# Kernel tuning notes

Measured on AMD Instinct MI355X. Metric: run time of the kernel, lower is better.

Reference implementation:

```python
import jax, jax.numpy as jnp
import numpy as np

EMBED_DIM = 512
NUM_HEADS = 8
HEAD_DIM = EMBED_DIM // NUM_HEADS
B, N, M = 4, 4096, 4096


def setup_inputs() -> dict:
    key = jax.random.key(0)
    ks = jax.random.split(key, 16)
    s = 0.02
    inp = {
        "query": jax.random.normal(ks[0], (B, N, EMBED_DIM), jnp.float32),
        "key": jax.random.normal(ks[1], (B, M, EMBED_DIM), jnp.float32),
        "value": jax.random.normal(ks[2], (B, M, EMBED_DIM), jnp.float32),
        # Linear weights stored as (in, out) so y = x @ W + b (== torch x @ W.T + b)
        "Wq": jax.random.normal(ks[3], (EMBED_DIM, EMBED_DIM), jnp.float32) * s,
        "bq": jnp.zeros((EMBED_DIM,), jnp.float32),
        "Wk": jax.random.normal(ks[4], (EMBED_DIM, EMBED_DIM), jnp.float32) * s,
        "bk": jnp.zeros((EMBED_DIM,), jnp.float32),
        "Wv": jax.random.normal(ks[5], (EMBED_DIM, EMBED_DIM), jnp.float32) * s,
        "bv": jnp.zeros((EMBED_DIM,), jnp.float32),
        # rank expansion MLP acts per-head on head_dim
        "W1": jax.random.normal(ks[6], (HEAD_DIM, HEAD_DIM * 2), jnp.float32) * s,
        "b1": jnp.zeros((HEAD_DIM * 2,), jnp.float32),
        "W2": jax.random.normal(ks[7], (HEAD_DIM * 2, HEAD_DIM), jnp.float32) * s,
        "b2": jnp.zeros((HEAD_DIM,), jnp.float32),
        "Wo": jax.random.normal(ks[8], (EMBED_DIM, EMBED_DIM), jnp.float32) * s,
        "bo": jnp.zeros((EMBED_DIM,), jnp.float32),
    }
    return inp


def reference(query, key, value, Wq, bq, Wk, bk, Wv, bv, W1, b1, W2, b2, Wo, bo):
    b, n, _ = query.shape
    m = key.shape[1]
    H, D = NUM_HEADS, HEAD_DIM
    # ELU+1 feature maps on projected q, k
    q = jax.nn.elu(query @ Wq + bq) + 1.0           # [B,N,E]
    k = jax.nn.elu(key @ Wk + bk) + 1.0             # [B,M,E]
    v = value @ Wv + bv                              # [B,M,E]
    q = q.reshape(b, n, H, D)
    k = k.reshape(b, m, H, D)
    v = v.reshape(b, m, H, D)
    # rank expansion MLP on keys (per head_dim), exact GELU as nn.GELU default
    k_aug = jax.nn.gelu(k @ W1 + b1, approximate=False) @ W2 + b2
    k_aug = jax.nn.elu(k_aug) + 1.0                  # [B,M,H,D]
    # inputs already fp32 (torch .float() casts are identity here)
    k_scaled = k_aug / m                             # normalize over context len
    kv_context = jnp.einsum('bmhd,bmhe->bhde', k_scaled, v)   # [B,H,D,D]
    out = jnp.einsum('bnhd,bhde->bnhe', q, kv_context)        # [B,N,H,D]
    k_sum = k_scaled.sum(axis=1)                      # [B,H,D]
    denom = jnp.einsum('bnhd,bhd->bnh', q, k_sum)     # [B,N,H]
    out = out / jnp.clip(denom, 1e-6, None)[..., None]
    out = jnp.clip(jnp.nan_to_num(out, nan=0.0, posinf=65000.0, neginf=-65000.0),
                   -65000.0, 65000.0)
    out = out.reshape(b, n, H * D)
    return out @ Wo + bo
```

## Files before the change

kernel.cpp:

```cpp
#include <hip/hip_runtime.h>
#include <cmath>

#define DEV __device__ __forceinline__

typedef __bf16 bf16x8 __attribute__((ext_vector_type(8)));
typedef float f32x4 __attribute__((ext_vector_type(4)));
typedef unsigned int u32;
typedef unsigned short u16;

DEV u16 f2bf(float f) {
  union { float f; u32 u; } v;
  v.f = f;
  u32 u = v.u;
  u += 0x7fffu + ((u >> 16) & 1u);
  return (u16)(u >> 16);
}

DEV void async16(const void* g, void* l) {
  __builtin_amdgcn_global_load_lds((const __attribute__((address_space(1))) u32*)g,
                                   (__attribute__((address_space(3))) u32*)l, 16, 0, 0);
}

enum { ACT_ID = 0, ACT_ELU1 = 1, ACT_GELU = 2, ACT_ELU1S = 3 };
enum { OM_ROW = 0, OM_VT = 1 };

DEV float apply_act(int ACT, float v, float scale) {
  if (ACT == ACT_ELU1)  return (v > 0.f) ? (v + 1.f) : __expf(v);
  if (ACT == ACT_GELU)  return 0.5f * v * (1.f + erff(v * 0.7071067811865475f));
  if (ACT == ACT_ELU1S) return ((v > 0.f) ? (v + 1.f) : __expf(v)) * scale;
  return v;
}

template <int BM, int BN, int K, int WR, int WC, int ACT, int OBF16, int OMODE, int AFP32>
__global__ __launch_bounds__(256)
void gemm_bf16(const void* __restrict__ Av, const u16* __restrict__ Bt,
               const float* __restrict__ bias, void* __restrict__ Yv,
               int NC, float scale)
{
  constexpr int BI = BN / 64;
  constexpr int SBASE = BM * 32 + BN * 32;
  constexpr int SBSZ = (OMODE == OM_VT && 4 * 64 * 72 > SBASE) ? 4 * 64 * 72 : SBASE;
  __shared__ __align__(16) u16 SB[SBSZ];
  u16* AsU = SB;
  u16* Bs = SB + BM * 32;
  static_assert(WR * WC == 4, "4 waves");

  const int tid = threadIdx.x;
  const int wv = tid >> 6, lane = tid & 63;
  const int wr = wv / WC, wc = wv % WC;
  const int lrow = lane & 15, lq = lane >> 4;
  const int c0 = blockIdx.x * BN;
  const long r0 = (long)blockIdx.y * BM;
  const float* Af = (const float*)Av;
  const u16* Ah = (const u16*)Av;

  f32x4 acc[4][4] = {};

  for (int kt = 0; kt < K; kt += 32) {
    if (AFP32) {
      const int row = tid >> 2, kq = tid & 3;
#pragma unroll
      for (int it = 0; it < BM / 64; ++it) {
        const int r = it * 64 + row;
        const float* g = Af + (r0 + r) * K + kt + kq * 8;
        float4 lo = *(const float4*)g;
        float4 hi = *(const float4*)(g + 4);
        union { ushort4 h[2]; uint4 q; } pk;
        pk.h[0].x = f2bf(lo.x); pk.h[0].y = f2bf(lo.y);
        pk.h[0].z = f2bf(lo.z); pk.h[0].w = f2bf(lo.w);
        pk.h[1].x = f2bf(hi.x); pk.h[1].y = f2bf(hi.y);
        pk.h[1].z = f2bf(hi.z); pk.h[1].w = f2bf(hi.w);
        *(uint4*)&AsU[r * 32 + kq * 8] = pk.q;
      }
    } else {
#pragma unroll
      for (int i = 0; i < BM / 64; ++i) {
        const int s = (wv * (BM / 64) + i) * 64 + lane;
        async16(Ah + (r0 + (s >> 2)) * (long)K + kt + (s & 3) * 8,
                &AsU[(wv * (BM / 64) + i) * 512]);
      }
    }
#pragma unroll
    for (int i = 0; i < BI; ++i) {
      const int s = (wv * BI + i) * 64 + lane;
      async16(Bt + ((long)c0 + (s >> 2)) * K + kt + (s & 3) * 8,
              &Bs[(wv * BI + i) * 512]);
    }
    __syncthreads();
    bf16x8 af[4], bfr[4];
#pragma unroll
    for (int i = 0; i < 4; ++i)
      af[i] = *(const bf16x8*)&AsU[(wr * 64 + i * 16 + lrow) * 32 + lq * 8];
#pragma unroll
    for (int j = 0; j < 4; ++j)
      bfr[j] = *(const bf16x8*)&Bs[(wc * 64 + j * 16 + lrow) * 32 + lq * 8];
#pragma unroll
    for (int i = 0; i < 4; ++i)
#pragma unroll
      for (int j = 0; j < 4; ++j)
        acc[i][j] = __builtin_amdgcn_mfma_f32_16x16x32_bf16(af[i], bfr[j], acc[i][j], 0, 0, 0);
    __syncthreads();
  }

  float* Yf = (float*)Yv;
  u16* Yh = (u16*)Yv;

  if (OMODE == OM_ROW) {
#pragma unroll
    for (int i = 0; i < 4; ++i) {
#pragma unroll
      for (int j = 0; j < 4; ++j) {
        const int col = c0 + wc * 64 + j * 16 + lrow;
        const float bv = bias[col];
#pragma unroll
        for (int p = 0; p < 4; ++p) {
          const float o = apply_act(ACT, acc[i][j][p] + bv, scale);
          const long row = r0 + wr * 64 + i * 16 + lq * 4 + p;
          const long yi = row * NC + col;
          if (OBF16) Yh[yi] = f2bf(o);
          else       Yf[yi] = o;
        }
      }
    }
  } else {
    u16* LTv = SB + wv * 4608;
#pragma unroll
    for (int i = 0; i < 4; ++i) {
#pragma unroll
      for (int j = 0; j < 4; ++j) {
        const int col = c0 + wc * 64 + j * 16 + lrow;
        const float bv = bias[col];
        ushort4 w;
        w.x = f2bf(apply_act(ACT, acc[i][j][0] + bv, scale));
        w.y = f2bf(apply_act(ACT, acc[i][j][1] + bv, scale));
        w.z = f2bf(apply_act(ACT, acc[i][j][2] + bv, scale));
        w.w = f2bf(apply_act(ACT, acc[i][j][3] + bv, scale));
        const int e_l = j * 16 + lrow;
        const int m_l = i * 16 + lq * 4;
        *(ushort4*)&LTv[e_l * 72 + m_l] = w;
      }
    }
    const int b = (int)(r0 >> 12);
    const int h = (c0 + wc * 64) >> 6;
    const int mg0 = (int)(r0 & 4095) + wr * 64;
#pragma unroll
    for (int ps = 0; ps < 8; ++ps) {
      const int e = ps * 8 + (lane >> 3);
      const int mq = (lane & 7) * 8;
      uint4 v = *(const uint4*)&LTv[e * 72 + mq];
      *(uint4*)(Yh + (((long)b * 8 + h) * 64 + e) * 4096 + mg0 + mq) = v;
    }
  }
}

struct TArgs {
  const float* src[6];
  u16* dst[6];
  int K[6];
  int N[6];
};
__global__ __launch_bounds__(256)
void transpose_w(TArgs a)
{
  const int m = blockIdx.z;
  const int K = a.K[m], N = a.N[m];
  const int kt = blockIdx.y * 64, nt = blockIdx.x * 64;
  if (kt >= K || nt >= N) return;
  const float* src = a.src[m];
  u16* dst = a.dst[m];
  __shared__ u16 t[64][72];
  const int tx = threadIdx.x & 15, ty = threadIdx.x >> 4;
#pragma unroll
  for (int rr = 0; rr < 64; rr += 16) {
    const int k = kt + ty + rr;
    float4 v = *(const float4*)(src + (long)k * N + nt + tx * 4);
    t[tx * 4 + 0][ty + rr] = f2bf(v.x);
    t[tx * 4 + 1][ty + rr] = f2bf(v.y);
    t[tx * 4 + 2][ty + rr] = f2bf(v.z);
    t[tx * 4 + 3][ty + rr] = f2bf(v.w);
  }
  __syncthreads();
#pragma unroll
  for (int it = 0; it < 2; ++it) {
    const int s = threadIdx.x + it * 256;
    const int r = s >> 3, c = (s & 7) * 8;
    ushort4 u0 = *(ushort4*)&t[r][c];
    ushort4 u1 = *(ushort4*)&t[r][c + 4];
    *(ushort4*)(dst + (long)(nt + r) * K + kt + c) = u0;
    *(ushort4*)(dst + (long)(nt + r) * K + kt + c + 4) = u1;
  }
}

__global__ __launch_bounds__(256)
void mlp_fused(const u16* __restrict__ kact, const u16* __restrict__ W1T,
               const u16* __restrict__ W2T, const float* __restrict__ b1,
               const float* __restrict__ b2, u16* __restrict__ kaT, float invM)
{
  __shared__ __align__(16) u16 SB[27136];
  u16* As  = SB;
  u16* W1p = SB + 9216;
  u16* W2p = SB + 18432;
  u16* hid = SB;
  u16* LT2 = SB;

  const int tid = threadIdx.x, wv = tid >> 6, lane = tid & 63;
  const int lrow = lane & 15, lq = lane >> 4;
  const int bh = blockIdx.y, b = bh >> 3, h = bh & 7;
  const int m0 = blockIdx.x * 128;
  const long kbase = ((long)b * 4096 + m0) * 512 + h * 64;

#pragma unroll
  for (int i = 0; i < 4; ++i) {
    const int c = i * 256 + tid;
    const int row = c >> 3, p = c & 7;
    uint4 v = *(const uint4*)(kact + kbase + (long)row * 512 + p * 8);
    *(uint4*)&As[row * 72 + p * 8] = v;
  }
#pragma unroll
  for (int i = 0; i < 4; ++i) {
    const int c = i * 256 + tid;
    const int row = c >> 3, p = c & 7;
    uint4 v = *(const uint4*)(W1T + c * 8);
    *(uint4*)&W1p[row * 72 + p * 8] = v;
  }
#pragma unroll
  for (int i = 0; i < 4; ++i) {
    const int c = i * 256 + tid;
    const int row = c >> 4, p = c & 15;
    uint4 v = *(const uint4*)(W2T + c * 8);
    *(uint4*)&W2p[row * 136 + p * 8] = v;
  }
  __syncthreads();

  const int c0 = (wv >> 1) * 64, mh0 = (wv & 1) * 64;
  f32x4 acc1[4][4] = {};
#pragma unroll
  for (int kt = 0; kt < 2; ++kt) {
    bf16x8 wa[4], kb[4];
#pragma unroll
    for (int i = 0; i < 4; ++i)
      wa[i] = *(const bf16x8*)&W1p[(c0 + i * 16 + lrow) * 72 + kt * 32 + lq * 8];
#pragma unroll
    for (int j = 0; j < 4; ++j)
      kb[j] = *(const bf16x8*)&As[(mh0 + j * 16 + lrow) * 72 + kt * 32 + lq * 8];
#pragma unroll
    for (int i = 0; i < 4; ++i)
#pragma unroll
      for (int j = 0; j < 4; ++j)
        acc1[i][j] = __builtin_amdgcn_mfma_f32_16x16x32_bf16(wa[i], kb[j], acc1[i][j], 0, 0, 0);
  }
  __syncthreads();

#pragma unroll
  for (int i = 0; i < 4; ++i) {
    const int cc = c0 + i * 16 + lq * 4;
    float4 bv = *(const float4*)(b1 + cc);
#pragma unroll
    for (int j = 0; j < 4; ++j) {
      const int m = mh0 + j * 16 + lrow;
      float x0 = acc1[i][j][0] + bv.x, x1 = acc1[i][j][1] + bv.y;
      float x2 = acc1[i][j][2] + bv.z, x3 = acc1[i][j][3] + bv.w;
      ushort4 w;
      w.x = f2bf(0.5f * x0 * (1.f + erff(x0 * 0.7071067811865475f)));
      w.y = f2bf(0.5f * x1 * (1.f + erff(x1 * 0.7071067811865475f)));
      w.z = f2bf(0.5f * x2 * (1.f + erff(x2 * 0.7071067811865475f)));
      w.w = f2bf(0.5f * x3 * (1.f + erff(x3 * 0.7071067811865475f)));
      *(ushort4*)&hid[m * 136 + cc] = w;
    }
  }
  __syncthreads();

  const int d0 = (wv >> 1) * 32, mh2 = (wv & 1) * 64;
  f32x4 acc2[4][2] = {};
#pragma unroll
  for (int kt = 0; kt < 4; ++kt) {
    bf16x8 wa[2], hb[4];
#pragma unroll
    for (int i = 0; i < 2; ++i)
      wa[i] = *(const bf16x8*)&W2p[(d0 + i * 16 + lrow) * 136 + kt * 32 + lq * 8];
#pragma unroll
    for (int j = 0; j < 4; ++j)
      hb[j] = *(const bf16x8*)&hid[(mh2 + j * 16 + lrow) * 136 + kt * 32 + lq * 8];
#pragma unroll
    for (int j = 0; j < 4; ++j)
#pragma unroll
      for (int i = 0; i < 2; ++i)
        acc2[j][i] = __builtin_amdgcn_mfma_f32_16x16x32_bf16(hb[j], wa[i], acc2[j][i], 0, 0, 0);
  }
  __syncthreads();

#pragma unroll
  for (int i = 0; i < 2; ++i) {
    const int d = d0 + i * 16 + lrow;
    const float bd = b2[d];
#pragma unroll
    for (int j = 0; j < 4; ++j) {
      const int ml = mh2 + j * 16 + lq * 4;
      ushort4 w;
#pragma unroll
      for (int p = 0; p < 4; ++p) {
        float v = acc2[j][i][p] + bd;
        v = ((v > 0.f) ? (v + 1.f) : __expf(v)) * invM;
        ((u16*)&w)[p] = f2bf(v);
      }
      *(ushort4*)&LT2[d * 136 + ml] = w;
    }
  }
  __syncthreads();
#pragma unroll
  for (int it = 0; it < 4; ++it) {
    const int c = it * 256 + tid;
    const int d = c >> 4, mq = (c & 15) * 8;
    uint4 v = *(const uint4*)&LT2[d * 136 + mq];
    *(uint4*)(kaT + ((long)bh * 64 + d) * 4096 + m0 + mq) = v;
  }
}

__global__ __launch_bounds__(256)
void kv_gemm(const u16* __restrict__ kaT, const u16* __restrict__ vT,
             float* __restrict__ kvp, float* __restrict__ ksp)
{
  const int sp = blockIdx.x;
  const int bh = blockIdx.y;
  __shared__ u16 SB[16384];
  u16* As = SB;
  u16* Bs = SB + 8192;
  const int tid = threadIdx.x, wv = tid >> 6, lane = tid & 63;
  const int lrow = lane & 15, lq = lane >> 4;
  f32x4 acc[4][4] = {};
  f32x4 accs[4] = {};
  bf16x8 ones;
#pragma unroll
  for (int z = 0; z < 8; ++z) ones[z] = (__bf16)1.0f;
  const long base = (long)bh * 64 * 4096;

  for (int ph = 0; ph < 2; ++ph) {
    const int m0 = sp * 256 + ph * 128;
#pragma unroll
    for (int i = 0; i < 4; ++i) {
      const int s = (wv * 4 + i) * 64 + lane;
      const int chunk = s >> 8, row = (s >> 2) & 63, part = s & 3;
      const long g = base + (long)row * 4096 + m0 + chunk * 32 + part * 8;
      async16(kaT + g, &As[(wv * 4 + i) * 512]);
      async16(vT + g, &Bs[(wv * 4 + i) * 512]);
    }
    __syncthreads();
    bf16x8 af[4], bfr[4];
#pragma unroll
    for (int i = 0; i < 4; ++i)
      af[i] = *(const bf16x8*)&As[wv * 2048 + (i * 16 + lrow) * 32 + lq * 8];
#pragma unroll
    for (int j = 0; j < 4; ++j)
      bfr[j] = *(const bf16x8*)&Bs[wv * 2048 + (j * 16 + lrow) * 32 + lq * 8];
#pragma unroll
    for (int i = 0; i < 4; ++i) {
#pragma unroll
      for (int j = 0; j < 4; ++j)
        acc[i][j] = __builtin_amdgcn_mfma_f32_16x16x32_bf16(af[i], bfr[j], acc[i][j], 0, 0, 0);
      accs[i] = __builtin_amdgcn_mfma_f32_16x16x32_bf16(af[i], ones, accs[i], 0, 0, 0);
    }
    __syncthreads();
  }

  float* red = (float*)SB;
  float* ksr = red + 64 * 68;
  for (int w = 0; w < 4; ++w) {
    __syncthreads();
    if (wv == w) {
#pragma unroll
      for (int i = 0; i < 4; ++i) {
#pragma unroll
        for (int j = 0; j < 4; ++j) {
          const int e = j * 16 + lrow, dd = i * 16 + lq * 4;
          float* p = &red[e * 68 + dd];
          if (w == 0) { p[0] = acc[i][j][0]; p[1] = acc[i][j][1]; p[2] = acc[i][j][2]; p[3] = acc[i][j][3]; }
          else        { p[0] += acc[i][j][0]; p[1] += acc[i][j][1]; p[2] += acc[i][j][2]; p[3] += acc[i][j][3]; }
        }
        if (lrow == 0) {
          const int dd = i * 16 + lq * 4;
#pragma unroll
          for (int p2 = 0; p2 < 4; ++p2) {
            if (w == 0) ksr[dd + p2] = accs[i][p2];
            else        ksr[dd + p2] += accs[i][p2];
          }
        }
      }
    }
  }
  __syncthreads();
  float* kvo = kvp + ((long)sp * 32 + bh) * 4096;
  for (int s = tid; s < 4096; s += 256) kvo[s] = red[(s >> 6) * 68 + (s & 63)];
  if (tid < 64) ksp[(sp * 32 + bh) * 64 + tid] = ksr[tid];
}

__global__ __launch_bounds__(256)
void kv_reduce(const float* __restrict__ kvp, const float* __restrict__ ksp,
               u16* __restrict__ kvT, u16* __restrict__ ksumT)
{
  const int bh = blockIdx.x;
  const int t = threadIdx.x;
  for (int s = t; s < 4096; s += 256) {
    float v = 0.f;
#pragma unroll
    for (int sp = 0; sp < 16; ++sp) v += kvp[((long)sp * 32 + bh) * 4096 + s];
    kvT[(long)bh * 4096 + s] = f2bf(v);
  }
  if (t < 64) {
    float v = 0.f;
#pragma unroll
    for (int sp = 0; sp < 16; ++sp) v += ksp[(sp * 32 + bh) * 64 + t];
    ksumT[bh * 64 + t] = f2bf(v);
  }
}

__global__ __launch_bounds__(256)
void attn_mfma(const u16* __restrict__ q, const u16* __restrict__ kvT,
               const u16* __restrict__ ksumT, u16* __restrict__ attn)
{
  __shared__ u16 SB[17408];
  const int tid = threadIdx.x, wv = tid >> 6, lane = tid & 63;
  const int lrow = lane & 15, lq = lane >> 4;
  const int n0 = blockIdx.x * 256;
  const int bh = blockIdx.y, b = bh >> 3, h = bh & 7;
  u16* As = SB;

#pragma unroll
  for (int half = 0; half < 2; ++half)
#pragma unroll
    for (int i = 0; i < 4; ++i) {
      const int s = (wv * 4 + i) * 64 + lane;
      async16(q + ((long)(b * 4096 + n0 + (s >> 2))) * 512 + h * 64 + half * 32 + (s & 3) * 8,
              &As[half * 8192 + (wv * 4 + i) * 512]);
    }
  bf16x8 bfr[2][4], ks[2];
#pragma unroll
  for (int half = 0; half < 2; ++half) {
#pragma unroll
    for (int j = 0; j < 4; ++j)
      bfr[half][j] = *(const bf16x8*)(kvT + ((long)bh * 64 + j * 16 + lrow) * 64 + half * 32 + lq * 8);
    ks[half] = *(const bf16x8*)(ksumT + bh * 64 + half * 32 + lq * 8);
  }
  __syncthreads();

  f32x4 acc[4][4] = {};
  f32x4 accd[4] = {};
#pragma unroll
  for (int half = 0; half < 2; ++half) {
    bf16x8 af[4];
#pragma unroll
    for (int i = 0; i < 4; ++i)
      af[i] = *(const bf16x8*)&As[half * 8192 + (wv * 64 + i * 16 + lrow) * 32 + lq * 8];
#pragma unroll
    for (int i = 0; i < 4; ++i) {
#pragma unroll
      for (int j = 0; j < 4; ++j)
        acc[i][j] = __builtin_amdgcn_mfma_f32_16x16x32_bf16(af[i], bfr[half][j], acc[i][j], 0, 0, 0);
      accd[i] = __builtin_amdgcn_mfma_f32_16x16x32_bf16(af[i], ks[half], accd[i], 0, 0, 0);
    }
  }
  __syncthreads();

  u16* LT = SB;
#pragma unroll
  for (int i = 0; i < 4; ++i) {
    float dinv[4];
#pragma unroll
    for (int p = 0; p < 4; ++p) dinv[p] = 1.f / fmaxf(accd[i][p], 1e-6f);
#pragma unroll
    for (int j = 0; j < 4; ++j) {
      const int e = j * 16 + lrow;
      const int nl0 = i * 16 + lq * 4;
      ushort4 w;
      float x0 = acc[i][j][0] * dinv[0], x1 = acc[i][j][1] * dinv[1];
      float x2 = acc[i][j][2] * dinv[2], x3 = acc[i][j][3] * dinv[3];
      if (!(x0 == x0)) x0 = 0.f;
      if (!(x1 == x1)) x1 = 0.f;
      if (!(x2 == x2)) x2 = 0.f;
      if (!(x3 == x3)) x3 = 0.f;
      w.x = f2bf(fminf(65000.f, fmaxf(-65000.f, x0)));
      w.y = f2bf(fminf(65000.f, fmaxf(-65000.f, x1)));
      w.z = f2bf(fminf(65000.f, fmaxf(-65000.f, x2)));
      w.w = f2bf(fminf(65000.f, fmaxf(-65000.f, x3)));
      *(ushort4*)&LT[wv * 4352 + e * 68 + nl0] = w;
    }
  }
  __syncthreads();
#pragma unroll
  for (int it = 0; it < 8; ++it) {
    const int c = it * 256 + tid;
    const int n = c & 255, ec = c >> 8;
    const int wr2 = n >> 6, nl = n & 63;
    ushort4 w0, w1;
    w0.x = LT[wr2 * 4352 + (ec * 8 + 0) * 68 + nl];
    w0.y = LT[wr2 * 4352 + (ec * 8 + 1) * 68 + nl];
    w0.z = LT[wr2 * 4352 + (ec * 8 + 2) * 68 + nl];
    w0.w = LT[wr2 * 4352 + (ec * 8 + 3) * 68 + nl];
    w1.x = LT[wr2 * 4352 + (ec * 8 + 4) * 68 + nl];
    w1.y = LT[wr2 * 4352 + (ec * 8 + 5) * 68 + nl];
    w1.z = LT[wr2 * 4352 + (ec * 8 + 6) * 68 + nl];
    w1.w = LT[wr2 * 4352 + (ec * 8 + 7) * 68 + nl];
    u16* dst = attn + ((long)(b * 4096 + n0 + n)) * 512 + h * 64 + ec * 8;
    *(ushort4*)dst = w0;
    *(ushort4*)(dst + 4) = w1;
  }
}

static constexpr long U = 8388608;

extern "C" void kernel_launch(void* const* d_in, const int* in_sizes, int n_in,
                              void* d_out, int out_size, void* d_ws, size_t ws_size,
                              hipStream_t stream)
{
  const float* query = (const float*)d_in[0];
  const float* key   = (const float*)d_in[1];
  const float* value = (const float*)d_in[2];
  const float* Wq = (const float*)d_in[3];
  const float* bq = (const float*)d_in[4];
  const float* Wk = (const float*)d_in[5];
  const float* bk = (const float*)d_in[6];
  const float* Wv = (const float*)d_in[7];
  const float* bv = (const float*)d_in[8];
  const float* W1 = (const float*)d_in[9];
  const float* b1 = (const float*)d_in[10];
  const float* W2 = (const float*)d_in[11];
  const float* b2 = (const float*)d_in[12];
  const float* Wo = (const float*)d_in[13];
  const float* bo = (const float*)d_in[14];

  u16* wsh = (u16*)d_ws;
  u16* qact = wsh;
  u16* kact = wsh + U;
  u16* vT   = wsh + 2 * U;
  u16* kaT  = wsh + 3 * U;
  u16* attn = wsh + 4 * U;

  float* fp  = (float*)(wsh + 5 * U);
  float* kvp = fp;
  float* ksp = fp + 2097152;
  u16* kvTg   = (u16*)(fp + 2129920);
  u16* ksumTg = kvTg + 131072;
  u16* wtb = ksumTg + 2048;
  u16* WqT = wtb;
  u16* WkT = wtb + 262144;
  u16* WvT = wtb + 524288;
  u16* WoT = wtb + 786432;
  u16* W1T = wtb + 1048576;
  u16* W2T = wtb + 1056768;

  dim3 blk(256);
  const float invM = 1.f / 4096.f;

  TArgs ta;
  ta.src[0] = Wq; ta.dst[0] = WqT; ta.K[0] = 512; ta.N[0] = 512;
  ta.src[1] = Wk; ta.dst[1] = WkT; ta.K[1] = 512; ta.N[1] = 512;
  ta.src[2] = Wv; ta.dst[2] = WvT; ta.K[2] = 512; ta.N[2] = 512;
  ta.src[3] = Wo; ta.dst[3] = WoT; ta.K[3] = 512; ta.N[3] = 512;
  ta.src[4] = W1; ta.dst[4] = W1T; ta.K[4] = 64;  ta.N[4] = 128;
  ta.src[5] = W2; ta.dst[5] = W2T; ta.K[5] = 128; ta.N[5] = 64;
  transpose_w<<<dim3(8, 8, 6), blk, 0, stream>>>(ta);

  gemm_bf16<128,128,512,2,2,ACT_ELU1,1,OM_ROW,1><<<dim3(4,128), blk, 0, stream>>>(query, WqT, bq, qact, 512, 1.f);
  gemm_bf16<128,128,512,2,2,ACT_ELU1,1,OM_ROW,1><<<dim3(4,128), blk, 0, stream>>>(key,   WkT, bk, kact, 512, 1.f);
  gemm_bf16<128,128,512,2,2,ACT_ID,  1,OM_VT, 1><<<dim3(4,128), blk, 0, stream>>>(value, WvT, bv, vT,   512, 1.f);
  mlp_fused<<<dim3(32,32), blk, 0, stream>>>(kact, W1T, W2T, b1, b2, kaT, invM);
  kv_gemm<<<dim3(16,32), blk, 0, stream>>>(kaT, vT, kvp, ksp);
  kv_reduce<<<dim3(32), blk, 0, stream>>>(kvp, ksp, kvTg, ksumTg);
  attn_mfma<<<dim3(16,32), blk, 0, stream>>>(qact, kvTg, ksumTg, attn);
  gemm_bf16<128,128,512,2,2,ACT_ID,0,OM_ROW,0><<<dim3(4,128), blk, 0, stream>>>(attn, WoT, bo, (float*)d_out, 512, 1.f);
}
```

Measured before the change: 305.9 us.

## Merge QKV projections into one launch with async fp32 loads to LDS

```diff
diff --git a/kernel.cpp b/kernel.cpp
--- a/kernel.cpp
+++ b/kernel.cpp
@@ -1,4 +1,5 @@
 #include <hip/hip_runtime.h>
+#include <hip/hip_bf16.h>
 #include <cmath>
 
 #define DEV __device__ __forceinline__
@@ -15,82 +16,69 @@
   u += 0x7fffu + ((u >> 16) & 1u);
   return (u16)(u >> 16);
 }
+DEV u32 pk2(float a, float b) {
+  union { __hip_bfloat162 h2; u32 u; } v;
+  v.h2 = __float22bfloat162_rn(float2{a, b});
+  return v.u;
+}
 
 DEV void async16(const void* g, void* l) {
   __builtin_amdgcn_global_load_lds((const __attribute__((address_space(1))) u32*)g,
                                    (__attribute__((address_space(3))) u32*)l, 16, 0, 0);
 }
 
-enum { ACT_ID = 0, ACT_ELU1 = 1, ACT_GELU = 2, ACT_ELU1S = 3 };
-enum { OM_ROW = 0, OM_VT = 1 };
-
-DEV float apply_act(int ACT, float v, float scale) {
-  if (ACT == ACT_ELU1)  return (v > 0.f) ? (v + 1.f) : __expf(v);
-  if (ACT == ACT_GELU)  return 0.5f * v * (1.f + erff(v * 0.7071067811865475f));
-  if (ACT == ACT_ELU1S) return ((v > 0.f) ? (v + 1.f) : __expf(v)) * scale;
-  return v;
-}
-
-template <int BM, int BN, int K, int WR, int WC, int ACT, int OBF16, int OMODE, int AFP32>
 __global__ __launch_bounds__(256)
-void gemm_bf16(const void* __restrict__ Av, const u16* __restrict__ Bt,
-               const float* __restrict__ bias, void* __restrict__ Yv,
-               int NC, float scale)
-{
-  constexpr int BI = BN / 64;
-  constexpr int SBASE = BM * 32 + BN * 32;
-  constexpr int SBSZ = (OMODE == OM_VT && 4 * 64 * 72 > SBASE) ? 4 * 64 * 72 : SBASE;
-  __shared__ __align__(16) u16 SB[SBSZ];
-  u16* AsU = SB;
-  u16* Bs = SB + BM * 32;
-  static_assert(WR * WC == 4, "4 waves");
-
-  const int tid = threadIdx.x;
-  const int wv = tid >> 6, lane = tid & 63;
-  const int wr = wv / WC, wc = wv % WC;
+void qkv_gemm(const float* __restrict__ qin, const float* __restrict__ kin,
+              const float* __restrict__ vin, const u16* __restrict__ WqT,
+              const u16* __restrict__ WkT, const u16* __restrict__ WvT,
+              const float* __restrict__ bq, const float* __restrict__ bk,
+              const float* __restrict__ bv, u16* __restrict__ qact,
+              u16* __restrict__ kact, u16* __restrict__ vT)
+{
+  __shared__ __align__(16) u16 SB[18432];
+  float* Asf = (float*)SB;
+  u16* Bs = SB + 8192;
+
+  const int z = blockIdx.z;
+  const float* Af = z == 0 ? qin : z == 1 ? kin : vin;
+  const u16* Bt = z == 0 ? WqT : z == 1 ? WkT : WvT;
+  const float* bias = z == 0 ? bq : z == 1 ? bk : bv;
+
+  const int tid = threadIdx.x, wv = tid >> 6, lane = tid & 63;
+  const int wr = wv >> 1, wc = wv & 1;
   const int lrow = lane & 15, lq = lane >> 4;
-  const int c0 = blockIdx.x * BN;
-  const long r0 = (long)blockIdx.y * BM;
-  const float* Af = (const float*)Av;
-  const u16* Ah = (const u16*)Av;
+  const long r0 = (long)blockIdx.x * 128;
+  const int c0 = blockIdx.y * 128;
 
   f32x4 acc[4][4] = {};
 
-  for (int kt = 0; kt < K; kt += 32) {
-    if (AFP32) {
-      const int row = tid >> 2, kq = tid & 3;
-#pragma unroll
-      for (int it = 0; it < BM / 64; ++it) {
-        const int r = it * 64 + row;
-        const float* g = Af + (r0 + r) * K + kt + kq * 8;
-        float4 lo = *(const float4*)g;
-        float4 hi = *(const float4*)(g + 4);
-        union { ushort4 h[2]; uint4 q; } pk;
-        pk.h[0].x = f2bf(lo.x); pk.h[0].y = f2bf(lo.y);
-        pk.h[0].z = f2bf(lo.z); pk.h[0].w = f2bf(lo.w);
-        pk.h[1].x = f2bf(hi.x); pk.h[1].y = f2bf(hi.y);
-        pk.h[1].z = f2bf(hi.z); pk.h[1].w = f2bf(hi.w);
-        *(uint4*)&AsU[r * 32 + kq * 8] = pk.q;
-      }
-    } else {
-#pragma unroll
-      for (int i = 0; i < BM / 64; ++i) {
-        const int s = (wv * (BM / 64) + i) * 64 + lane;
-        async16(Ah + (r0 + (s >> 2)) * (long)K + kt + (s & 3) * 8,
-                &AsU[(wv * (BM / 64) + i) * 512]);
-      }
-    }
-#pragma unroll
-    for (int i = 0; i < BI; ++i) {
-      const int s = (wv * BI + i) * 64 + lane;
-      async16(Bt + ((long)c0 + (s >> 2)) * K + kt + (s & 3) * 8,
-              &Bs[(wv * BI + i) * 512]);
+  for (int kt = 0; kt < 512; kt += 32) {
+#pragma unroll
+    for (int i = 0; i < 4; ++i) {
+      const int s = (wv * 4 + i) * 64 + lane;
+      const int row = s >> 3, p = s & 7;
+      const int gp = p ^ (row & 7);
+      async16(Af + (r0 + row) * 512 + kt + gp * 4, (char*)SB + (wv * 4 + i) * 1024);
+    }
+#pragma unroll
+    for (int i = 0; i < 2; ++i) {
+      const int s = (wv * 2 + i) * 64 + lane;
+      async16(Bt + ((long)c0 + (s >> 2)) * 512 + kt + (s & 3) * 8,
+              &Bs[(wv * 2 + i) * 512]);
     }
     __syncthreads();
     bf16x8 af[4], bfr[4];
 #pragma unroll
-    for (int i = 0; i < 4; ++i)
-      af[i] = *(const bf16x8*)&AsU[(wr * 64 + i * 16 + lrow) * 32 + lq * 8];
+    for (int i = 0; i < 4; ++i) {
+      const int r = wr * 64 + i * 16 + lrow;
+      const int r7 = r & 7, P0 = lq * 2;
+      float4 lo = *(const float4*)&Asf[r * 32 + (P0 ^ r7) * 4];
+      float4 hi = *(const float4*)&Asf[r * 32 + ((P0 + 1) ^ r7) * 4];
+      union { u32 q[4]; bf16x8 v; } pk;
+      pk.q[0] = pk2(lo.x, lo.y); pk.q[1] = pk2(lo.z, lo.w);
+      pk.q[2] = pk2(hi.x, hi.y); pk.q[3] = pk2(hi.z, hi.w);
+      af[i] = pk.v;
+    }
 #pragma unroll
     for (int j = 0; j < 4; ++j)
       bfr[j] = *(const bf16x8*)&Bs[(wc * 64 + j * 16 + lrow) * 32 + lq * 8];
@@ -102,23 +90,20 @@
     __syncthreads();
   }
 
-  float* Yf = (float*)Yv;
-  u16* Yh = (u16*)Yv;
-
-  if (OMODE == OM_ROW) {
+  if (z < 2) {
+    u16* Y = z == 0 ? qact : kact;
 #pragma unroll
     for (int i = 0; i < 4; ++i) {
 #pragma unroll
       for (int j = 0; j < 4; ++j) {
         const int col = c0 + wc * 64 + j * 16 + lrow;
-        const float bv = bias[col];
+        const float bvv = bias[col];
 #pragma unroll
         for (int p = 0; p < 4; ++p) {
-          const float o = apply_act(ACT, acc[i][j][p] + bv, scale);
+          float o = acc[i][j][p] + bvv;
+          o = (o > 0.f) ? (o + 1.f) : __expf(o);
           const long row = r0 + wr * 64 + i * 16 + lq * 4 + p;
-          const long yi = row * NC + col;
-          if (OBF16) Yh[yi] = f2bf(o);
-          else       Yf[yi] = o;
+          Y[row * 512 + col] = f2bf(o);
         }
       }
     }
@@ -129,15 +114,13 @@
 #pragma unroll
       for (int j = 0; j < 4; ++j) {
         const int col = c0 + wc * 64 + j * 16 + lrow;
-        const float bv = bias[col];
+        const float bvv = bias[col];
         ushort4 w;
-        w.x = f2bf(apply_act(ACT, acc[i][j][0] + bv, scale));
-        w.y = f2bf(apply_act(ACT, acc[i][j][1] + bv, scale));
-        w.z = f2bf(apply_act(ACT, acc[i][j][2] + bv, scale));
-        w.w = f2bf(apply_act(ACT, acc[i][j][3] + bv, scale));
-        const int e_l = j * 16 + lrow;
-        const int m_l = i * 16 + lq * 4;
-        *(ushort4*)&LTv[e_l * 72 + m_l] = w;
+        w.x = f2bf(acc[i][j][0] + bvv);
+        w.y = f2bf(acc[i][j][1] + bvv);
+        w.z = f2bf(acc[i][j][2] + bvv);
+        w.w = f2bf(acc[i][j][3] + bvv);
+        *(ushort4*)&LTv[(j * 16 + lrow) * 72 + i * 16 + lq * 4] = w;
       }
     }
     const int b = (int)(r0 >> 12);
@@ -148,7 +131,58 @@
       const int e = ps * 8 + (lane >> 3);
       const int mq = (lane & 7) * 8;
       uint4 v = *(const uint4*)&LTv[e * 72 + mq];
-      *(uint4*)(Yh + (((long)b * 8 + h) * 64 + e) * 4096 + mg0 + mq) = v;
+      *(uint4*)(vT + (((long)b * 8 + h) * 64 + e) * 4096 + mg0 + mq) = v;
+    }
+  }
+}
+
+__global__ __launch_bounds__(256)
+void out_gemm(const u16* __restrict__ A, const u16* __restrict__ Bt,
+              const float* __restrict__ bias, float* __restrict__ Y)
+{
+  __shared__ __align__(16) u16 SB[8192];
+  u16* As = SB;
+  u16* Bs = SB + 4096;
+  const int tid = threadIdx.x, wv = tid >> 6, lane = tid & 63;
+  const int wr = wv >> 1, wc = wv & 1;
+  const int lrow = lane & 15, lq = lane >> 4;
+  const long r0 = (long)blockIdx.x * 128;
+  const int c0 = blockIdx.y * 128;
+
+  f32x4 acc[4][4] = {};
+  for (int kt = 0; kt < 512; kt += 32) {
+#pragma unroll
+    for (int i = 0; i < 2; ++i) {
+      const int s = (wv * 2 + i) * 64 + lane;
+      async16(A + (r0 + (s >> 2)) * 512 + kt + (s & 3) * 8, &As[(wv * 2 + i) * 512]);
+      async16(Bt + ((long)c0 + (s >> 2)) * 512 + kt + (s & 3) * 8, &Bs[(wv * 2 + i) * 512]);
+    }
+    __syncthreads();
+    bf16x8 af[4], bfr[4];
+#pragma unroll
+    for (int i = 0; i < 4; ++i)
+      af[i] = *(const bf16x8*)&As[(wr * 64 + i * 16 + lrow) * 32 + lq * 8];
+#pragma unroll
+    for (int j = 0; j < 4; ++j)
+      bfr[j] = *(const bf16x8*)&Bs[(wc * 64 + j * 16 + lrow) * 32 + lq * 8];
+#pragma unroll
+    for (int i = 0; i < 4; ++i)
+#pragma unroll
+      for (int j = 0; j < 4; ++j)
+        acc[i][j] = __builtin_amdgcn_mfma_f32_16x16x32_bf16(af[i], bfr[j], acc[i][j], 0, 0, 0);
+    __syncthreads();
+  }
+#pragma unroll
+  for (int i = 0; i < 4; ++i) {
+#pragma unroll
+    for (int j = 0; j < 4; ++j) {
+      const int col = c0 + wc * 64 + j * 16 + lrow;
+      const float bv = bias[col];
+#pragma unroll
+      for (int p = 0; p < 4; ++p) {
+        const long row = r0 + wr * 64 + i * 16 + lq * 4 + p;
+        Y[row * 512 + col] = acc[i][j][p] + bv;
+      }
     }
   }
 }
@@ -559,12 +593,11 @@
   ta.src[5] = W2; ta.dst[5] = W2T; ta.K[5] = 128; ta.N[5] = 64;
   transpose_w<<<dim3(8, 8, 6), blk, 0, stream>>>(ta);
 
-  gemm_bf16<128,128,512,2,2,ACT_ELU1,1,OM_ROW,1><<<dim3(4,128), blk, 0, stream>>>(query, WqT, bq, qact, 512, 1.f);
-  gemm_bf16<128,128,512,2,2,ACT_ELU1,1,OM_ROW,1><<<dim3(4,128), blk, 0, stream>>>(key,   WkT, bk, kact, 512, 1.f);
-  gemm_bf16<128,128,512,2,2,ACT_ID,  1,OM_VT, 1><<<dim3(4,128), blk, 0, stream>>>(value, WvT, bv, vT,   512, 1.f);
-  mlp_fused<<<dim3(32,32), blk, 0, stream>>>(kact, W1T, W2T, b1, b2, kaT, invM);
-  kv_gemm<<<dim3(16,32), blk, 0, stream>>>(kaT, vT, kvp, ksp);
+  qkv_gemm<<<dim3(128, 4, 3), blk, 0, stream>>>(query, key, value, WqT, WkT, WvT,
+                                                bq, bk, bv, qact, kact, vT);
+  mlp_fused<<<dim3(32, 32), blk, 0, stream>>>(kact, W1T, W2T, b1, b2, kaT, invM);
+  kv_gemm<<<dim3(16, 32), blk, 0, stream>>>(kaT, vT, kvp, ksp);
   kv_reduce<<<dim3(32), blk, 0, stream>>>(kvp, ksp, kvTg, ksumTg);
-  attn_mfma<<<dim3(16,32), blk, 0, stream>>>(qact, kvTg, ksumTg, attn);
-  gemm_bf16<128,128,512,2,2,ACT_ID,0,OM_ROW,0><<<dim3(4,128), blk, 0, stream>>>(attn, WoT, bo, (float*)d_out, 512, 1.f);
-}
+  attn_mfma<<<dim3(16, 32), blk, 0, stream>>>(qact, kvTg, ksumTg, attn);
+  out_gemm<<<dim3(128, 4), blk, 0, stream>>>(attn, WoT, bo, (float*)d_out);
+}
```

Measured after the change: 276.9 us. 1.1x faster.
